# Performance work log

Hardware: AMD Instinct MI355X
Metric: run time of the kernel (lower is better)

## Reference

```python
import jax, jax.numpy as jnp
import numpy as np

EPS = 1e-15

def _artanh(x):
    return jnp.arctanh(jnp.clip(x, -1 + 1e-7, 1 - 1e-7))

def mobius_matvec(M, x, c=1.0):
    # Poincare ball Mobius matrix-vector product (geoopt convention), c=1.
    sqc = jnp.sqrt(c)
    xn = jnp.maximum(jnp.linalg.norm(x, axis=-1, keepdims=True), EPS)
    mx = x @ M.T
    mxn = jnp.maximum(jnp.linalg.norm(mx, axis=-1, keepdims=True), EPS)
    return jnp.tanh(mxn / xn * _artanh(sqc * xn)) * mx / (mxn * sqc)

def mobius_add(x, y, c=1.0):
    x2 = jnp.sum(x * x, axis=-1, keepdims=True)
    y2 = jnp.sum(y * y, axis=-1, keepdims=True)
    xy = jnp.sum(x * y, axis=-1, keepdims=True)
    num = (1 + 2 * c * xy + c * y2) * x + (1 - c * x2) * y
    den = 1 + 2 * c * xy + (c ** 2) * x2 * y2
    return num / (den + EPS)

def hyp_linear(x, W, b):
    return mobius_add(mobius_matvec(W, x), b)

def hyperbolic_scores(q, k):
    # q,k: [B,H,S,D], elementwise clamp_max as in source
    q = jnp.minimum(q, 1 - 1e-5)
    k = jnp.minimum(k, 1 - 1e-5)
    q2 = jnp.sum(q * q, axis=-1, keepdims=True)          # [B,H,S,1]
    k2 = jnp.sum(k * k, axis=-1, keepdims=True)          # [B,H,S,1]
    qk = jnp.einsum('bhqd,bhkd->bhqk', q, k)             # [B,H,S,S]
    numer = 2 * (q2 + jnp.swapaxes(k2, -2, -1) - 2 * qk)
    denom = (1 - q2) * jnp.swapaxes(1 - k2, -2, -1) + EPS
    dist_sq = jnp.arccosh(jnp.maximum(1 + numer / denom, 1.0))
    dist_sq = jnp.maximum(dist_sq, 1e-7)
    return -dist_sq

def reference(x, Wq, bq, Wk, bk, Wv, bv, Wo, bo, head_scaling):
    B, S, E = x.shape
    H = head_scaling.shape[0]
    D = E // H
    q = hyp_linear(x, Wq, bq).reshape(B, S, H, D).transpose(0, 2, 1, 3)
    k = hyp_linear(x, Wk, bk).reshape(B, S, H, D).transpose(0, 2, 1, 3)
    v = hyp_linear(x, Wv, bv).reshape(B, S, H, D).transpose(0, 2, 1, 3)
    scores = hyperbolic_scores(q, k) / (head_scaling * (D ** 0.5))  # [B,H,S,S]
    w = jax.nn.softmax(scores, axis=-1)
    out = jnp.einsum('bhqk,bhkd->bhqd', w, v)
    out = out.transpose(0, 2, 1, 3).reshape(B, S, E)
    return hyp_linear(out, Wo, bo)

def setup_inputs() -> dict:
    key = jax.random.key(0)
    ks = jax.random.split(key, 6)
    B, S, E, H = 8, 1024, 768, 12
    x = jax.random.normal(ks[0], (B, S, E), dtype=jnp.float32) * 0.05
    Wq = jax.random.normal(ks[1], (E, E), dtype=jnp.float32) * 0.05
    Wk = jax.random.normal(ks[2], (E, E), dtype=jnp.float32) * 0.05
    Wv = jax.random.normal(ks[3], (E, E), dtype=jnp.float32) * 0.05
    Wo = jax.random.normal(ks[4], (E, E), dtype=jnp.float32) * 0.05
    z = jnp.zeros((E,), dtype=jnp.float32)
    return {'x': x, 'Wq': Wq, 'bq': z, 'Wk': Wk, 'bk': z, 'Wv': Wv, 'bv': z,
            'Wo': Wo, 'bo': z, 'head_scaling': jnp.ones((H, 1, 1), dtype=jnp.float32)}
```

## Files before the change

kernel.cpp:

```cpp
#include <hip/hip_runtime.h>
#include <hip/hip_bf16.h>
#include <math.h>

#define Bb 8
#define Ss 1024
#define Ee 768
#define Hh 12
#define Mm (Bb*Ss)
#define NW (Ee*Ee)
#define LQKV 2304

typedef short  s16x8 __attribute__((ext_vector_type(8)));
typedef float  f32x4 __attribute__((ext_vector_type(4)));

#define FENCE() __builtin_amdgcn_sched_barrier(0)
#define BAR_ONLY() do { FENCE(); __builtin_amdgcn_s_barrier(); FENCE(); } while(0)
#define BAR_LGKM() do { FENCE(); asm volatile("s_waitcnt lgkmcnt(0)" ::: "memory"); FENCE(); \
                        __builtin_amdgcn_s_barrier(); FENCE(); } while(0)

__device__ __forceinline__ unsigned short f2bf(float f) {
    __hip_bfloat16 b = __float2bfloat16(f);
    return *reinterpret_cast<unsigned short*>(&b);
}
__device__ __forceinline__ float bf2f(unsigned short h) {
    return __uint_as_float(((unsigned)h) << 16);
}

__device__ __forceinline__ float block_sum_256(float v, float* red) {
    #pragma unroll
    for (int off = 32; off > 0; off >>= 1) v += __shfl_down(v, off, 64);
    __syncthreads();
    if ((threadIdx.x & 63) == 0) red[threadIdx.x >> 6] = v;
    __syncthreads();
    return red[0] + red[1] + red[2] + red[3];
}

__global__ __launch_bounds__(256) void pack_xw_kernel(const float* __restrict__ x,
    const float* __restrict__ W0, const float* __restrict__ W1,
    const float* __restrict__ W2, const float* __restrict__ W3,
    unsigned short* __restrict__ Xb, float* __restrict__ xn,
    unsigned short* __restrict__ Wb) {
    __shared__ float red[4];
    const int bid = blockIdx.x;
    if (bid < Mm) {
        size_t row = bid;
        const float* a = x + row * Ee;
        float ssum = 0.f;
        #pragma unroll
        for (int l = 0; l < 3; ++l) {
            float v = a[threadIdx.x + l*256];
            ssum += v*v;
            Xb[row*Ee + threadIdx.x + l*256] = f2bf(v);
        }
        float tot = block_sum_256(ssum, red);
        if (threadIdx.x == 0) xn[row] = fmaxf(sqrtf(tot), 1e-15f);
    } else {
        int idx = bid - Mm;
        const int perW = NW/1024;
        int which = idx / perW;
        int chunk = idx - which*perW;
        const float* src = (which == 0) ? W0 : (which == 1) ? W1 : (which == 2) ? W2 : W3;
        size_t off = (size_t)chunk * 1024 + threadIdx.x * 4;
        float4 v = *reinterpret_cast<const float4*>(&src[off]);
        uint2 o;
        o.x = (unsigned)f2bf(v.x) | ((unsigned)f2bf(v.y) << 16);
        o.y = (unsigned)f2bf(v.z) | ((unsigned)f2bf(v.w) << 16);
        *reinterpret_cast<uint2*>(Wb + (size_t)which * NW + off) = o;
    }
}

template<int OUT16>
__global__ __launch_bounds__(256) void gemm_bf16_nt(const unsigned short* __restrict__ A,
                                                    int lda,
                                                    const unsigned short* __restrict__ B,
                                                    void* __restrict__ Cout, int ldc) {
    __shared__ alignas(16) unsigned short As[128][64];
    __shared__ alignas(16) unsigned short Bs[128][64];
    const int tid = threadIdx.x, lane = tid & 63, w = tid >> 6;
    const int g = lane >> 4, lg = lane & 15;
    const int mBase = blockIdx.x * 128, nBase = blockIdx.y * 128;
    const int wr = w >> 1, wc = w & 1;
    const int rr = tid >> 3, cc = tid & 7;
    const int csw = (cc ^ (rr & 7)) * 8;
    f32x4 zero4 = {0.f,0.f,0.f,0.f};
    f32x4 acc[4][4];
    #pragma unroll
    for (int i = 0; i < 4; ++i)
        #pragma unroll
        for (int j = 0; j < 4; ++j) acc[i][j] = zero4;

    s16x8 av[4], bv[4];
    #define GLOAD(k0) do { \
        _Pragma("unroll") \
        for (int i = 0; i < 4; ++i) { \
            av[i] = *(const s16x8*)&A[(size_t)(mBase + rr + i*32)*lda + (k0) + cc*8]; \
            bv[i] = *(const s16x8*)&B[(size_t)(nBase + rr + i*32)*Ee  + (k0) + cc*8]; \
        } } while(0)

    GLOAD(0);
    for (int k0 = 0; k0 < Ee; k0 += 64) {
        BAR_ONLY();
        #pragma unroll
        for (int i = 0; i < 4; ++i) {
            *(s16x8*)&As[rr + i*32][csw] = av[i];
            *(s16x8*)&Bs[rr + i*32][csw] = bv[i];
        }
        if (k0 + 64 < Ee) GLOAD(k0 + 64);
        BAR_LGKM();
        __builtin_amdgcn_s_setprio(1);
        #pragma unroll
        for (int kk = 0; kk < 2; ++kk) {
            s16x8 af[4], bfr[4];
            #pragma unroll
            for (int mi = 0; mi < 4; ++mi) {
                int ar = wr*64 + mi*16 + lg;
                af[mi] = *(const s16x8*)&As[ar][(((kk*4 + g) ^ (ar & 7)))*8];
            }
            #pragma unroll
            for (int ni = 0; ni < 4; ++ni) {
                int br = wc*64 + ni*16 + lg;
                bfr[ni] = *(const s16x8*)&Bs[br][(((kk*4 + g) ^ (br & 7)))*8];
            }
            #pragma unroll
            for (int mi = 0; mi < 4; ++mi)
                #pragma unroll
                for (int ni = 0; ni < 4; ++ni)
                    acc[mi][ni] = __builtin_amdgcn_mfma_f32_16x16x32_bf16(af[mi], bfr[ni], acc[mi][ni], 0, 0, 0);
        }
        __builtin_amdgcn_s_setprio(0);
    }
    #undef GLOAD
    #pragma unroll
    for (int mi = 0; mi < 4; ++mi)
        #pragma unroll
        for (int ni = 0; ni < 4; ++ni)
            #pragma unroll
            for (int r = 0; r < 4; ++r) {
                size_t off = (size_t)(mBase + wr*64 + mi*16 + g*4 + r)*ldc + nBase + wc*64 + ni*16 + lg;
                if (OUT16) ((unsigned short*)Cout)[off] = f2bf(acc[mi][ni][r]);
                else       ((float*)Cout)[off] = acc[mi][ni][r];
            }
}

__global__ __launch_bounds__(256) void fix_qkv_kernel(unsigned short* __restrict__ QKV,
                                                      const float* __restrict__ xn_buf,
                                                      const float* __restrict__ bq,
                                                      const float* __restrict__ bk,
                                                      const float* __restrict__ bv_,
                                                      float2* __restrict__ qinfo,
                                                      float2* __restrict__ kinfo) {
    __shared__ float red[4], red2[4];
    const int which = blockIdx.y;
    size_t row = blockIdx.x;
    const int tid = threadIdx.x;
    const float* bias = (which == 0) ? bq : (which == 1) ? bk : bv_;
    unsigned short* m = QKV + row * LQKV + which * Ee;
    float mv[3], bv[3];
    float ss = 0.f;
    #pragma unroll
    for (int l = 0; l < 3; ++l) { mv[l] = bf2f(m[tid + l*256]); ss += mv[l]*mv[l]; }
    float mxn2 = block_sum_256(ss, red);
    float mxn = fmaxf(sqrtf(mxn2), 1e-15f);
    float xn = xn_buf[row];
    float xc = fminf(xn, 1.f - 1e-7f);
    float at = 0.5f * logf((1.f + xc) / (1.f - xc));
    float th = tanhf(mxn / xn * at);
    float scale = th / mxn;
    float m2 = th * th;
    float mb = 0.f, b2 = 0.f;
    #pragma unroll
    for (int l = 0; l < 3; ++l) {
        bv[l] = bias[tid + l*256];
        mv[l] *= scale;
        mb += mv[l]*bv[l];
        b2 += bv[l]*bv[l];
    }
    mb = block_sum_256(mb, red);
    b2 = block_sum_256(b2, red2);
    float ncoef = 1.f + 2.f*mb + b2;
    float bcoef = 1.f - m2;
    float inv = 1.f / (1.f + 2.f*mb + m2*b2 + 1e-15f);
    const int lane = tid & 63, wv = tid >> 6;
    if (which < 2) {
        #pragma unroll
        for (int l = 0; l < 3; ++l) {
            float f = (ncoef*mv[l] + bcoef*bv[l]) * inv;
            float c = fminf(f, 1.f - 1e-5f);
            m[tid + l*256] = f2bf(c);
            float s2 = c*c;
            #pragma unroll
            for (int off = 1; off < 64; off <<= 1) s2 += __shfl_xor(s2, off);
            if (lane == 0) {
                if (which == 0)
                    qinfo[(size_t)(wv + 4*l)*Mm + row] = make_float2(2.f*s2, 1.f/(1.f - s2));
                else {
                    float ik = 1.f/(1.f - s2);
                    kinfo[(size_t)(wv + 4*l)*Mm + row] = make_float2(ik, 2.f*s2*ik);
                }
            }
        }
    } else {
        #pragma unroll
        for (int l = 0; l < 3; ++l)
            m[tid + l*256] = f2bf((ncoef*mv[l] + bcoef*bv[l]) * inv);
    }
}

__global__ __launch_bounds__(256) void transpose_v_kernel(const unsigned short* __restrict__ QKV,
                                                          unsigned short* __restrict__ Vb) {
    __shared__ unsigned short t[64][72];
    const int tid = threadIdx.x;
    const int st = blockIdx.x, h = blockIdx.y, b = blockIdx.z;
    {
        int sr = tid >> 2, d0 = (tid & 3) * 16;
        const unsigned short* vp = QKV + ((size_t)b*Ss + st*64 + sr)*LQKV + 2*Ee + h*64 + d0;
        *(s16x8*)&t[sr][d0]     = *(const s16x8*)&vp[0];
        *(s16x8*)&t[sr][d0 + 8] = *(const s16x8*)&vp[8];
    }
    __syncthreads();
    {
        int d = tid >> 2, s0 = (tid & 3) * 16;
        unsigned hu[8];
        #pragma unroll
        for (int i = 0; i < 8; ++i)
            hu[i] = (unsigned)t[s0 + 2*i][d] | ((unsigned)t[s0 + 2*i + 1][d] << 16);
        size_t obase = (((size_t)b*Hh + h)*64 + d)*Ss + st*64 + s0;
        *reinterpret_cast<uint4*>(&Vb[obase])     = make_uint4(hu[0],hu[1],hu[2],hu[3]);
        *reinterpret_cast<uint4*>(&Vb[obase + 8]) = make_uint4(hu[4],hu[5],hu[6],hu[7]);
    }
}

__global__ __launch_bounds__(256) void attn_mfma5(
    unsigned short* __restrict__ QKV, const unsigned short* __restrict__ Vb,
    const float2* __restrict__ qinfo, const float2* __restrict__ kinfo,
    const float* __restrict__ hs, float* __restrict__ osq)
{
    __shared__ alignas(16) unsigned short KHs[2][64][64];
    __shared__ alignas(16) unsigned short VHs[2][64][64];
    __shared__ alignas(16) unsigned short PHs[4][2][16][64];
    __shared__ float us[2][64], vs[2][64];

    const int tid = threadIdx.x, lane = tid & 63, w = tid >> 6;
    const int g = lane >> 4, lg = lane & 15;
    const int qt = blockIdx.x, h = blockIdx.y, b = blockIdx.z;
    const int q0 = qt * 128, hoff = h * 64;
    const size_t rowB = (size_t)b * Ss;
    const size_t hMm = (size_t)h * Mm;
    const size_t vBase = (((size_t)b*Hh + h)*64)*Ss;
    const int rr = tid >> 3, cc = tid & 7;
    const int csw = (cc ^ (rr & 7)) * 8;

    const unsigned short* kgp = &QKV[(rowB + rr)*LQKV + Ee + hoff + cc*8];
    const unsigned short* vgp = &Vb[vBase + (size_t)rr*Ss + cc*8];

    s16x8 qh[2][2];
    float a2s[2], ioms[2];
    #pragma unroll
    for (int qi = 0; qi < 2; ++qi) {
        const unsigned short* qp = QKV + (rowB + q0 + 32*w + qi*16 + lg)*LQKV + hoff;
        qh[qi][0] = *(const s16x8*)&qp[g*8];
        qh[qi][1] = *(const s16x8*)&qp[32 + g*8];
        float2 qiv = qinfo[hMm + rowB + q0 + 32*w + qi*16 + lg];
        a2s[qi] = qiv.x;
        ioms[qi] = qiv.y;
    }
    const float nia = -1.f / (hs[h] * 8.f);

    s16x8 cka, ckb, cva, cvb, nka, nkb, nva, nvb;
    #define LOADKV(ka,kb,va,vb_,kt) do { \
        ka  = *(const s16x8*)&kgp[(size_t)(kt)*64*LQKV]; \
        kb  = *(const s16x8*)&kgp[(size_t)(kt)*64*LQKV + (size_t)32*LQKV]; \
        va  = *(const s16x8*)&vgp[(kt)*64]; \
        vb_ = *(const s16x8*)&vgp[(size_t)32*Ss + (kt)*64]; } while(0)
    #define WRITEKV(bi,ka,kb,va,vb_) do { \
        *(s16x8*)&KHs[bi][rr     ][csw] = ka; \
        *(s16x8*)&KHs[bi][rr + 32][csw] = kb; \
        *(s16x8*)&VHs[bi][rr     ][csw] = va; \
        *(s16x8*)&VHs[bi][rr + 32][csw] = vb_; } while(0)

    LOADKV(cka,ckb,cva,cvb, 0);
    LOADKV(nka,nkb,nva,nvb, 1);
    float2 uvC = make_float2(0.f,0.f), uvN = make_float2(0.f,0.f);
    if (tid < 64) uvC = kinfo[hMm + rowB + tid];
    if (tid < 64) uvN = kinfo[hMm + rowB + 64 + tid];
    WRITEKV(0, cka,ckb,cva,cvb);
    if (tid < 64) { us[0][tid] = uvC.x; vs[0][tid] = uvC.y; }
    BAR_LGKM();

    f32x4 zero4 = {0.f,0.f,0.f,0.f};
    f32x4 oacc[2][4];
    #pragma unroll
    for (int qi = 0; qi < 2; ++qi)
        #pragma unroll
        for (int i = 0; i < 4; ++i) oacc[qi][i] = zero4;
    float lsum0 = 0.f, lsum1 = 0.f;
    int cur = 0;

    for (int kt = 0; kt < 16; ++kt) {
        if (kt < 15) {
            WRITEKV(cur^1, nka,nkb,nva,nvb);
            if (tid < 64) { us[cur^1][tid] = uvN.x; vs[cur^1][tid] = uvN.y; }
        }
        if (kt < 14) {
            LOADKV(nka,nkb,nva,nvb, kt+2);
            if (tid < 64) uvN = kinfo[hMm + rowB + (kt+2)*64 + tid];
        }

        f32x4 sacc[2][4];
        #pragma unroll
        for (int qi = 0; qi < 2; ++qi)
            #pragma unroll
            for (int i = 0; i < 4; ++i) sacc[qi][i] = zero4;
        __builtin_amdgcn_s_setprio(1);
        #pragma unroll
        for (int nt = 0; nt < 4; ++nt) {
            const int krow = nt*16 + lg, sw = krow & 7;
            s16x8 kh0 = *(const s16x8*)&KHs[cur][krow][((g    ) ^ sw)*8];
            s16x8 kh1 = *(const s16x8*)&KHs[cur][krow][((4 + g) ^ sw)*8];
            sacc[0][nt] = __builtin_amdgcn_mfma_f32_16x16x32_bf16(kh0, qh[0][0], sacc[0][nt], 0, 0, 0);
            sacc[0][nt] = __builtin_amdgcn_mfma_f32_16x16x32_bf16(kh1, qh[0][1], sacc[0][nt], 0, 0, 0);
            sacc[1][nt] = __builtin_amdgcn_mfma_f32_16x16x32_bf16(kh0, qh[1][0], sacc[1][nt], 0, 0, 0);
            sacc[1][nt] = __builtin_amdgcn_mfma_f32_16x16x32_bf16(kh1, qh[1][1], sacc[1][nt], 0, 0, 0);
        }
        __builtin_amdgcn_s_setprio(0);

        #pragma unroll
        for (int nt = 0; nt < 4; ++nt) {
            const int j0 = nt*16 + g*4;
            float4 uq4 = *reinterpret_cast<const float4*>(&us[cur][j0]);
            float4 vq4 = *reinterpret_cast<const float4*>(&vs[cur][j0]);
            float uqa[4] = {uq4.x, uq4.y, uq4.z, uq4.w};
            float vqa[4] = {vq4.x, vq4.y, vq4.z, vq4.w};
            const int chq = ((j0 >> 3) ^ (lg & 7))*8 + (j0 & 7);
            #pragma unroll
            for (int qi = 0; qi < 2; ++qi) {
                float pr[4];
                #pragma unroll
                for (int r = 0; r < 4; ++r) {
                    float s  = sacc[qi][nt][r];
                    float wv = fmaf(-4.f, s, a2s[qi]);
                    float z  = fmaf(ioms[qi], fmaf(uqa[r], wv, vqa[r]), 1.f);
                    z = fmaxf(z, 1.f);
                    float sq = __builtin_amdgcn_sqrtf(fmaf(z, z, -1.f));
                    float uu = z + sq;
                    float p  = __builtin_amdgcn_exp2f(nia * __builtin_amdgcn_logf(uu));
                    if (qi == 0) lsum0 += p; else lsum1 += p;
                    pr[r] = p;
                }
                unsigned p01, p23;
                asm("v_cvt_pk_bf16_f32 %0, %1, %2" : "=v"(p01) : "v"(pr[0]), "v"(pr[1]));
                asm("v_cvt_pk_bf16_f32 %0, %1, %2" : "=v"(p23) : "v"(pr[2]), "v"(pr[3]));
                *reinterpret_cast<uint2*>(&PHs[w][qi][lg][chq]) = make_uint2(p01, p23);
            }
        }

        __builtin_amdgcn_s_setprio(1);
        #pragma unroll
        for (int jh = 0; jh < 2; ++jh) {
            s16x8 pa0 = *(const s16x8*)&PHs[w][0][lg][((jh*4 + g) ^ (lg & 7))*8];
            s16x8 pa1 = *(const s16x8*)&PHs[w][1][lg][((jh*4 + g) ^ (lg & 7))*8];
            #pragma unroll
            for (int nt2 = 0; nt2 < 4; ++nt2) {
                const int vrow = nt2*16 + lg;
                s16x8 vh = *(const s16x8*)&VHs[cur][vrow][((jh*4 + g) ^ (vrow & 7))*8];
                oacc[0][nt2] = __builtin_amdgcn_mfma_f32_16x16x32_bf16(pa0, vh, oacc[0][nt2], 0, 0, 0);
                oacc[1][nt2] = __builtin_amdgcn_mfma_f32_16x16x32_bf16(pa1, vh, oacc[1][nt2], 0, 0, 0);
            }
        }
        __builtin_amdgcn_s_setprio(0);

        BAR_LGKM();
        cur ^= 1;
    }
    #undef LOADKV
    #undef WRITEKV

    #pragma unroll
    for (int qi = 0; qi < 2; ++qi) {
        float ls = (qi == 0) ? lsum0 : lsum1;
        ls += __shfl_xor(ls, 16);
        ls += __shfl_xor(ls, 32);
        #pragma unroll
        for (int r = 0; r < 4; ++r) {
            float lr = __shfl(ls, g*4 + r, 64);
            float li = 1.f / lr;
            float sq = 0.f;
            const size_t orow = rowB + q0 + 32*w + qi*16 + g*4 + r;
            #pragma unroll
            for (int nt2 = 0; nt2 < 4; ++nt2) {
                float o = oacc[qi][nt2][r] * li;
                sq = fmaf(o, o, sq);
                QKV[orow*LQKV + 2*Ee + hoff + nt2*16 + lg] = f2bf(o);
            }
            sq += __shfl_xor(sq, 1);
            sq += __shfl_xor(sq, 2);
            sq += __shfl_xor(sq, 4);
            sq += __shfl_xor(sq, 8);
            if (lg == 0) osq[hMm + orow] = sq;
        }
    }
}

__global__ __launch_bounds__(256) void mobius_fix_final(const float* __restrict__ src,
                                                        float* __restrict__ dst,
                                                        const float* __restrict__ osq,
                                                        const float* __restrict__ bias) {
    __shared__ float red[4], red2[4];
    size_t row = blockIdx.x;
    const float* m = src + row * Ee;
    float mv[3], bv[3];
    float ss = 0.f;
    #pragma unroll
    for (int l = 0; l < 3; ++l) { mv[l] = m[threadIdx.x + l*256]; ss += mv[l]*mv[l]; }
    float mxn2 = block_sum_256(ss, red);
    float mxn = fmaxf(sqrtf(mxn2), 1e-15f);
    float ss2 = 0.f;
    #pragma unroll
    for (int hh = 0; hh < Hh; ++hh) ss2 += osq[(size_t)hh*Mm + row];
    float xn = fmaxf(sqrtf(ss2), 1e-15f);
    float xc = fminf(xn, 1.f - 1e-7f);
    float at = 0.5f * logf((1.f + xc) / (1.f - xc));
    float th = tanhf(mxn / xn * at);
    float scale = th / mxn;
    float m2 = th * th;
    float mb = 0.f, b2 = 0.f;
    #pragma unroll
    for (int l = 0; l < 3; ++l) {
        bv[l] = bias[threadIdx.x + l*256];
        mv[l] *= scale;
        mb += mv[l]*bv[l];
        b2 += bv[l]*bv[l];
    }
    mb = block_sum_256(mb, red);
    b2 = block_sum_256(b2, red2);
    float ncoef = 1.f + 2.f*mb + b2;
    float bcoef = 1.f - m2;
    float inv = 1.f / (1.f + 2.f*mb + m2*b2 + 1e-15f);
    float* d = dst + row * Ee;
    #pragma unroll
    for (int l = 0; l < 3; ++l)
        d[threadIdx.x + l*256] = (ncoef*mv[l] + bcoef*bv[l]) * inv;
}

extern "C" void kernel_launch(void* const* d_in, const int* in_sizes, int n_in,
                              void* d_out, int out_size, void* d_ws, size_t ws_size,
                              hipStream_t stream) {
    const float* x  = (const float*)d_in[0];
    const float* Wq = (const float*)d_in[1];
    const float* bq = (const float*)d_in[2];
    const float* Wk = (const float*)d_in[3];
    const float* bk = (const float*)d_in[4];
    const float* Wv = (const float*)d_in[5];
    const float* bv = (const float*)d_in[6];
    const float* Wo = (const float*)d_in[7];
    const float* bo = (const float*)d_in[8];
    const float* hs = (const float*)d_in[9];
    float* out = (float*)d_out;

    const size_t NE = (size_t)Mm * Ee;
    float* ws    = (float*)d_ws;
    float* xn_x  = ws;
    float* osq   = xn_x + Mm;
    float2* qinfo = (float2*)(osq + (size_t)Hh*Mm);
    float2* kinfo = qinfo + (size_t)Hh*Mm;
    unsigned short* qkvbf = (unsigned short*)(kinfo + (size_t)Hh*Mm);
    unsigned short* vtbf  = qkvbf + (size_t)Mm * LQKV;
    unsigned short* xbf   = vtbf + NE;
    unsigned short* wbf   = xbf + NE;
    float* fbuf = (float*)vtbf;

    pack_xw_kernel<<<Mm + 4*(NW/1024), 256, 0, stream>>>(x, Wq, Wk, Wv, Wo, xbf, xn_x, wbf);

    gemm_bf16_nt<1><<<dim3(Mm/128, LQKV/128), 256, 0, stream>>>(xbf, Ee, wbf, qkvbf, LQKV);
    fix_qkv_kernel<<<dim3(Mm, 3), 256, 0, stream>>>(qkvbf, xn_x, bq, bk, bv, qinfo, kinfo);
    transpose_v_kernel<<<dim3(Ss/64, Hh, Bb), 256, 0, stream>>>(qkvbf, vtbf);

    attn_mfma5<<<dim3(Ss/128, Hh, Bb), 256, 0, stream>>>(qkvbf, vtbf, qinfo, kinfo, hs, osq);

    gemm_bf16_nt<0><<<dim3(Mm/128, Ee/128), 256, 0, stream>>>(qkvbf + 2*Ee, LQKV, wbf + 3*(size_t)NW, fbuf, Ee);
    mobius_fix_final<<<Mm, 256, 0, stream>>>(fbuf, out, osq, bo);
}
```

Before: 207.0 us.

## Use direct global-to-LDS loads and XCD-aware block swizzle in bf16 GEMM

The GEMM now loads its tiles with global_load_lds, which writes straight into shared memory and skips the register staging and separate LDS stores. The grid is flattened to 1D and remapped so that consecutive blocks on each XCD cover nearby tiles, which should improve L2 reuse. In exchange it drops the XOR bank swizzle, so LDS reads may hit bank conflicts. It also loses the register prefetch that overlapped the next tile's loads with the MFMAs, so each iteration now waits on vmcnt(0) before computing.

```diff
diff --git a/kernel.cpp b/kernel.cpp
--- a/kernel.cpp
+++ b/kernel.cpp
@@ -17,6 +17,12 @@
 #define BAR_ONLY() do { FENCE(); __builtin_amdgcn_s_barrier(); FENCE(); } while(0)
 #define BAR_LGKM() do { FENCE(); asm volatile("s_waitcnt lgkmcnt(0)" ::: "memory"); FENCE(); \
                         __builtin_amdgcn_s_barrier(); FENCE(); } while(0)
+
+__device__ __forceinline__ void gload_lds16(const void* g, void* l) {
+    __builtin_amdgcn_global_load_lds(
+        (const __attribute__((address_space(1))) void*)g,
+        (__attribute__((address_space(3))) void*)l, 16, 0, 0);
+}
 
 __device__ __forceinline__ unsigned short f2bf(float f) {
     __hip_bfloat16 b = __float2bfloat16(f);
@@ -73,15 +79,18 @@
 __global__ __launch_bounds__(256) void gemm_bf16_nt(const unsigned short* __restrict__ A,
                                                     int lda,
                                                     const unsigned short* __restrict__ B,
-                                                    void* __restrict__ Cout, int ldc) {
+                                                    void* __restrict__ Cout, int ldc,
+                                                    int mtiles) {
     __shared__ alignas(16) unsigned short As[128][64];
     __shared__ alignas(16) unsigned short Bs[128][64];
     const int tid = threadIdx.x, lane = tid & 63, w = tid >> 6;
     const int g = lane >> 4, lg = lane & 15;
-    const int mBase = blockIdx.x * 128, nBase = blockIdx.y * 128;
+    const int cpx = gridDim.x >> 3;
+    const int swz = (blockIdx.x & 7) * cpx + (blockIdx.x >> 3);
+    const int mBase = (swz % mtiles) * 128, nBase = (swz / mtiles) * 128;
     const int wr = w >> 1, wc = w & 1;
-    const int rr = tid >> 3, cc = tid & 7;
-    const int csw = (cc ^ (rr & 7)) * 8;
+    const int sr8 = lane >> 3;
+    const int scol = (lane & 7) * 8;
     f32x4 zero4 = {0.f,0.f,0.f,0.f};
     f32x4 acc[4][4];
     #pragma unroll
@@ -89,47 +98,34 @@
         #pragma unroll
         for (int j = 0; j < 4; ++j) acc[i][j] = zero4;
 
-    s16x8 av[4], bv[4];
-    #define GLOAD(k0) do { \
-        _Pragma("unroll") \
-        for (int i = 0; i < 4; ++i) { \
-            av[i] = *(const s16x8*)&A[(size_t)(mBase + rr + i*32)*lda + (k0) + cc*8]; \
-            bv[i] = *(const s16x8*)&B[(size_t)(nBase + rr + i*32)*Ee  + (k0) + cc*8]; \
-        } } while(0)
-
-    GLOAD(0);
     for (int k0 = 0; k0 < Ee; k0 += 64) {
-        BAR_ONLY();
         #pragma unroll
         for (int i = 0; i < 4; ++i) {
-            *(s16x8*)&As[rr + i*32][csw] = av[i];
-            *(s16x8*)&Bs[rr + i*32][csw] = bv[i];
-        }
-        if (k0 + 64 < Ee) GLOAD(k0 + 64);
-        BAR_LGKM();
-        __builtin_amdgcn_s_setprio(1);
+            const int r0 = w*32 + i*8;
+            gload_lds16(&A[(size_t)(mBase + r0 + sr8)*lda + k0 + scol], &As[r0][0]);
+            gload_lds16(&B[(size_t)(nBase + r0 + sr8)*Ee  + k0 + scol], &Bs[r0][0]);
+        }
+        FENCE();
+        asm volatile("s_waitcnt vmcnt(0)" ::: "memory");
+        FENCE();
+        __builtin_amdgcn_s_barrier();
         #pragma unroll
         for (int kk = 0; kk < 2; ++kk) {
             s16x8 af[4], bfr[4];
             #pragma unroll
-            for (int mi = 0; mi < 4; ++mi) {
-                int ar = wr*64 + mi*16 + lg;
-                af[mi] = *(const s16x8*)&As[ar][(((kk*4 + g) ^ (ar & 7)))*8];
-            }
-            #pragma unroll
-            for (int ni = 0; ni < 4; ++ni) {
-                int br = wc*64 + ni*16 + lg;
-                bfr[ni] = *(const s16x8*)&Bs[br][(((kk*4 + g) ^ (br & 7)))*8];
-            }
+            for (int mi = 0; mi < 4; ++mi)
+                af[mi] = *(const s16x8*)&As[wr*64 + mi*16 + lg][(kk*4 + g)*8];
+            #pragma unroll
+            for (int ni = 0; ni < 4; ++ni)
+                bfr[ni] = *(const s16x8*)&Bs[wc*64 + ni*16 + lg][(kk*4 + g)*8];
             #pragma unroll
             for (int mi = 0; mi < 4; ++mi)
                 #pragma unroll
                 for (int ni = 0; ni < 4; ++ni)
                     acc[mi][ni] = __builtin_amdgcn_mfma_f32_16x16x32_bf16(af[mi], bfr[ni], acc[mi][ni], 0, 0, 0);
         }
-        __builtin_amdgcn_s_setprio(0);
-    }
-    #undef GLOAD
+        BAR_LGKM();
+    }
     #pragma unroll
     for (int mi = 0; mi < 4; ++mi)
         #pragma unroll
@@ -471,12 +467,12 @@
 
     pack_xw_kernel<<<Mm + 4*(NW/1024), 256, 0, stream>>>(x, Wq, Wk, Wv, Wo, xbf, xn_x, wbf);
 
-    gemm_bf16_nt<1><<<dim3(Mm/128, LQKV/128), 256, 0, stream>>>(xbf, Ee, wbf, qkvbf, LQKV);
+    gemm_bf16_nt<1><<<(Mm/128)*(LQKV/128), 256, 0, stream>>>(xbf, Ee, wbf, qkvbf, LQKV, Mm/128);
     fix_qkv_kernel<<<dim3(Mm, 3), 256, 0, stream>>>(qkvbf, xn_x, bq, bk, bv, qinfo, kinfo);
     transpose_v_kernel<<<dim3(Ss/64, Hh, Bb), 256, 0, stream>>>(qkvbf, vtbf);
 
     attn_mfma5<<<dim3(Ss/128, Hh, Bb), 256, 0, stream>>>(qkvbf, vtbf, qinfo, kinfo, hs, osq);
 
-    gemm_bf16_nt<0><<<dim3(Mm/128, Ee/128), 256, 0, stream>>>(qkvbf + 2*Ee, LQKV, wbf + 3*(size_t)NW, fbuf, Ee);
+    gemm_bf16_nt<0><<<(Mm/128)*(Ee/128), 256, 0, stream>>>(qkvbf + 2*Ee, LQKV, wbf + 3*(size_t)NW, fbuf, Ee, Mm/128);
     mobius_fix_final<<<Mm, 256, 0, stream>>>(fbuf, out, osq, bo);
 }
```

Result: slower. 224.3 us (+8.4%).
